# Kernel optimization log

Hardware: AMD Instinct MI355X
Metric: run time of the kernel (lower is better)

Reference implementation:

```python
import jax, jax.numpy as jnp
import numpy as np

B, N, K = 4, 8192, 16
EMBED, HID, NCLS = 64, 128, 13
EPS = 1e-5


def _bn(x, g, b):
    # BatchNorm1d in training mode: stats over all points (B*N), per channel
    m = jnp.mean(x, axis=(0, 1), keepdims=True)
    v = jnp.var(x, axis=(0, 1), keepdims=True)
    return (x - m) * jax.lax.rsqrt(v + EPS) * g + b


def _knn_idx(pos, k):
    # pos: [B,N,3] -> k nearest neighbor indices per point (self excluded)
    sq = jnp.sum(pos * pos, -1)  # [B,N]
    d2 = sq[:, :, None] + sq[:, None, :] - 2.0 * jnp.einsum('bnd,bmd->bnm', pos, pos)
    n = pos.shape[1]
    d2 = d2 + jnp.eye(n, dtype=pos.dtype) * 1e10  # mask self (loop=False)
    _, idx = jax.lax.top_k(-d2, k)  # [B,N,k]
    return idx


def _pt_conv(x, pos, idx, w_lin, w_src, w_dst, pos_w, pos_b):
    # PyG PointTransformerConv: vector attention over neighbors (incl. self loop)
    Bc = x.shape[0]
    bidx = jnp.arange(Bc)[:, None, None]
    v = x @ w_lin          # value:  lin(x)
    a_src = x @ w_src      # lin_src(x)
    a_dst = x @ w_dst      # lin_dst(x)
    vj = v[bidx, idx]                      # [B,N,k1,C]
    aj = a_src[bidx, idx]                  # [B,N,k1,C]
    pj = pos[bidx, idx]                    # [B,N,k1,3]
    delta = (pos[:, :, None, :] - pj) @ pos_w + pos_b   # pos_nn(pos_i - pos_j)
    attn = jax.nn.softmax(a_dst[:, :, None, :] - aj + delta, axis=2)
    return jnp.sum(attn * (vj + delta), axis=2)  # sum aggregation


def setup_inputs() -> dict:
    key = jax.random.key(0)
    ks = jax.random.split(key, 20)

    def w(k, fan_in, fan_out):
        return (jax.random.normal(k, (fan_in, fan_out), jnp.float32) / np.sqrt(fan_in)).astype(jnp.float32)

    inp = {
        'points': jax.random.normal(ks[0], (B, N, 3), jnp.float32),
        'embed_w1': w(ks[1], 3, EMBED), 'embed_b1': jnp.zeros((EMBED,), jnp.float32),
        'bn1_g': jnp.ones((EMBED,), jnp.float32), 'bn1_b': jnp.zeros((EMBED,), jnp.float32),
        'embed_w2': w(ks[2], EMBED, EMBED), 'embed_b2': jnp.zeros((EMBED,), jnp.float32),
        'bne_g': jnp.ones((EMBED,), jnp.float32), 'bne_b': jnp.zeros((EMBED,), jnp.float32),
        'l0_lin': w(ks[3], EMBED, HID), 'l0_src': w(ks[4], EMBED, HID), 'l0_dst': w(ks[5], EMBED, HID),
        'l0_pos_w': w(ks[6], 3, HID), 'l0_pos_b': jnp.zeros((HID,), jnp.float32),
        'l0_bn_g': jnp.ones((HID,), jnp.float32), 'l0_bn_b': jnp.zeros((HID,), jnp.float32),
        'l1_lin': w(ks[7], HID, HID), 'l1_src': w(ks[8], HID, HID), 'l1_dst': w(ks[9], HID, HID),
        'l1_pos_w': w(ks[10], 3, HID), 'l1_pos_b': jnp.zeros((HID,), jnp.float32),
        'l1_bn_g': jnp.ones((HID,), jnp.float32), 'l1_bn_b': jnp.zeros((HID,), jnp.float32),
        'dec_w1': w(ks[11], HID, HID), 'dec_b1': jnp.zeros((HID,), jnp.float32),
        'dec_bn_g': jnp.ones((HID,), jnp.float32), 'dec_bn_b': jnp.zeros((HID,), jnp.float32),
        'dec_w2': w(ks[12], HID, NCLS), 'dec_b2': jnp.zeros((NCLS,), jnp.float32),
    }
    return inp


def reference(points, embed_w1, embed_b1, bn1_g, bn1_b, embed_w2, embed_b2,
              bne_g, bne_b,
              l0_lin, l0_src, l0_dst, l0_pos_w, l0_pos_b, l0_bn_g, l0_bn_b,
              l1_lin, l1_src, l1_dst, l1_pos_w, l1_pos_b, l1_bn_g, l1_bn_b,
              dec_w1, dec_b1, dec_bn_g, dec_bn_b, dec_w2, dec_b2):
    Bc, Nc, _ = points.shape
    # embedding MLP: Linear -> BN -> ReLU -> Linear, then BN -> ReLU
    h = points @ embed_w1 + embed_b1
    h = jax.nn.relu(_bn(h, bn1_g, bn1_b))
    h = h @ embed_w2 + embed_b2
    x = jax.nn.relu(_bn(h, bne_g, bne_b))
    # kNN graph (per batch), then append self loop (add_self_loops=True)
    idx = _knn_idx(points, K)
    self_idx = jnp.broadcast_to(jnp.arange(Nc)[None, :, None], (Bc, Nc, 1))
    idxf = jnp.concatenate([idx, self_idx], axis=-1)  # [B,N,K+1]
    x = jax.nn.relu(_bn(_pt_conv(x, points, idxf, l0_lin, l0_src, l0_dst, l0_pos_w, l0_pos_b), l0_bn_g, l0_bn_b))
    x = jax.nn.relu(_bn(_pt_conv(x, points, idxf, l1_lin, l1_src, l1_dst, l1_pos_w, l1_pos_b), l1_bn_g, l1_bn_b))
    # decoder MLP (dropout = identity at inference)
    h = jax.nn.relu(_bn(x @ dec_w1 + dec_b1, dec_bn_g, dec_bn_b))
    logits = h @ dec_w2 + dec_b2  # [B,N,num_classes]
    return logits
```

## Files before the change

### kernel.cpp

```cpp
#include <hip/hip_runtime.h>
#include <math.h>

#define BB 4
#define NN 8192
#define PP 32768
#define KNN 16

typedef float f32x2 __attribute__((ext_vector_type(2)));
typedef float f32x4 __attribute__((ext_vector_type(4)));

__device__ __forceinline__ f32x2 pk_mul(f32x2 a, f32x2 b) {
  f32x2 d; asm("v_pk_mul_f32 %0, %1, %2" : "=v"(d) : "v"(a), "v"(b)); return d;
}
__device__ __forceinline__ f32x2 pk_add(f32x2 a, f32x2 b) {
  f32x2 d; asm("v_pk_add_f32 %0, %1, %2" : "=v"(d) : "v"(a), "v"(b)); return d;
}

__global__ __launch_bounds__(256) void k_embed1(const float* __restrict__ pts,
    const float* __restrict__ w1, const float* __restrict__ b1, float* __restrict__ h1)
{
  int tid = threadIdx.x;
  int c = tid & 63, g = tid >> 6;
  float wx = w1[c], wy = w1[64 + c], wz = w1[128 + c], bc = b1[c];
  int base = blockIdx.x * 256;
  #pragma unroll 4
  for (int i = 0; i < 64; ++i) {
    int p = base + g + i * 4;
    float px = pts[p*3+0], py = pts[p*3+1], pz = pts[p*3+2];
    float h = fmaf(pz, wz, fmaf(py, wy, fmaf(px, wx, bc)));
    h1[(size_t)p*64 + c] = h;
  }
}

__global__ __launch_bounds__(256) void k_prep(const float* __restrict__ pts, float* __restrict__ pp)
{
  int t = blockIdx.x * 256 + threadIdx.x;
  int b = t >> 12, m = t & 4095;
  int c = m >> 6, l = m & 63;
  int jl = b * NN + c * 128 + l;
  int jh = jl + 64;
  float xl = pts[jl*3+0], yl = pts[jl*3+1], zl = pts[jl*3+2];
  float xh = pts[jh*3+0], yh = pts[jh*3+1], zh = pts[jh*3+2];
  float wl = __fadd_rn(__fadd_rn(__fmul_rn(xl,xl), __fmul_rn(yl,yl)), __fmul_rn(zl,zl));
  float wh = __fadd_rn(__fadd_rn(__fmul_rn(xh,xh), __fmul_rn(yh,yh)), __fmul_rn(zh,zh));
  float* o = pp + (size_t)t * 8;
  *(float4*)(o + 0) = make_float4(xl, xh, yl, yh);
  *(float4*)(o + 4) = make_float4(zl, zh, wl, wh);
}

template<int C>
__global__ __launch_bounds__(256) void k_stats(const float* __restrict__ src,
    float* __restrict__ gsum, float* __restrict__ gss)
{
  constexpr int GPB = 256 / C;
  int tid = threadIdx.x;
  int c = tid % C, g = tid / C;
  float s = 0.f, ss = 0.f;
  for (int p = blockIdx.x * GPB + g; p < PP; p += gridDim.x * GPB) {
    float v = src[(size_t)p*C + c];
    s += v; ss = fmaf(v, v, ss);
  }
  __shared__ float ls[256], lq[256];
  ls[tid] = s; lq[tid] = ss;
  __syncthreads();
  if (tid < C) {
    float a = 0.f, b2 = 0.f;
    #pragma unroll
    for (int i = 0; i < GPB; ++i) { a += ls[tid + i*C]; b2 += lq[tid + i*C]; }
    atomicAdd(gsum + tid, a);
    atomicAdd(gss + tid, b2);
  }
}

__global__ void k_finalize(int C, const float* __restrict__ gsum, const float* __restrict__ gss,
    const float* __restrict__ gg, const float* __restrict__ bb,
    float* __restrict__ sc, float* __restrict__ sh)
{
  int c = threadIdx.x;
  if (c >= C) return;
  float mean = gsum[c] * (1.0f / PP);
  float var  = gss[c] * (1.0f / PP) - mean * mean;
  float s = gg[c] / sqrtf(var + 1e-5f);
  sc[c] = s;
  sh[c] = bb[c] - mean * s;
}

template<int K, int COUT>
__global__ __launch_bounds__(256) void k_proj(const float* __restrict__ in,
    const float* __restrict__ sc, const float* __restrict__ sh,
    const float* __restrict__ W0, const float* __restrict__ W1, const float* __restrict__ W2,
    const float* __restrict__ B0, const float* __restrict__ B1, const float* __restrict__ B2,
    float* __restrict__ O0, float* __restrict__ O1, float* __restrict__ O2)
{
  constexpr int PTS = 64;
  constexpr int CW = 8;
  constexpr int CG = COUT / CW;
  constexpr int PW = PTS * CG / 256;
  const float* W  = (blockIdx.y == 0) ? W0 : (blockIdx.y == 1) ? W1 : W2;
  const float* Bb = (blockIdx.y == 0) ? B0 : (blockIdx.y == 1) ? B1 : B2;
  float*       O  = (blockIdx.y == 0) ? O0 : (blockIdx.y == 1) ? O1 : O2;
  __shared__ float xs[PTS][K + 1];
  int tid = threadIdx.x;
  int pbase = blockIdx.x * PTS;
  constexpr int T4 = PTS * K / 4;
  for (int i = tid; i < T4; i += 256) {
    int p = i / (K/4), k = (i % (K/4)) * 4;
    float4 v = *(const float4*)(in + (size_t)(pbase + p)*K + k);
    v.x = fmaxf(fmaf(v.x, sc[k+0], sh[k+0]), 0.f);
    v.y = fmaxf(fmaf(v.y, sc[k+1], sh[k+1]), 0.f);
    v.z = fmaxf(fmaf(v.z, sc[k+2], sh[k+2]), 0.f);
    v.w = fmaxf(fmaf(v.w, sc[k+3], sh[k+3]), 0.f);
    xs[p][k+0] = v.x; xs[p][k+1] = v.y; xs[p][k+2] = v.z; xs[p][k+3] = v.w;
  }
  __syncthreads();
  int cg = tid % CG, pg = tid / CG;
  int c0 = cg * CW, p0 = pg * PW;
  float acc[PW][CW];
  #pragma unroll
  for (int i = 0; i < PW; ++i) {
    #pragma unroll
    for (int j = 0; j < CW; ++j) acc[i][j] = 0.f;
  }
  #pragma unroll 4
  for (int k = 0; k < K; ++k) {
    float4 wa = *(const float4*)(W + (size_t)k*COUT + c0);
    float4 wb = *(const float4*)(W + (size_t)k*COUT + c0 + 4);
    #pragma unroll
    for (int i = 0; i < PW; ++i) {
      float x = xs[p0 + i][k];
      acc[i][0] = fmaf(x, wa.x, acc[i][0]);
      acc[i][1] = fmaf(x, wa.y, acc[i][1]);
      acc[i][2] = fmaf(x, wa.z, acc[i][2]);
      acc[i][3] = fmaf(x, wa.w, acc[i][3]);
      acc[i][4] = fmaf(x, wb.x, acc[i][4]);
      acc[i][5] = fmaf(x, wb.y, acc[i][5]);
      acc[i][6] = fmaf(x, wb.z, acc[i][6]);
      acc[i][7] = fmaf(x, wb.w, acc[i][7]);
    }
  }
  float bj[CW];
  #pragma unroll
  for (int j = 0; j < CW; ++j) bj[j] = Bb ? Bb[c0 + j] : 0.f;
  #pragma unroll
  for (int i = 0; i < PW; ++i) {
    float* op = O + (size_t)(pbase + p0 + i)*COUT + c0;
    *(float4*)(op)     = make_float4(acc[i][0]+bj[0], acc[i][1]+bj[1], acc[i][2]+bj[2], acc[i][3]+bj[3]);
    *(float4*)(op + 4) = make_float4(acc[i][4]+bj[4], acc[i][5]+bj[5], acc[i][6]+bj[6], acc[i][7]+bj[7]);
  }
}

__global__ __launch_bounds__(256) void k_knn(const float* __restrict__ pp, int* __restrict__ idxout)
{
  int lane = threadIdx.x & 63;
  int wv = (blockIdx.x * 256 + threadIdx.x) >> 6;
  int b = wv >> 13, q = wv & (NN - 1);
  const float* pb = pp + (size_t)b * (NN * 4);
  const float* pq =
      nullptr;
  int qc = q >> 7, qr = q & 127;
  {
  }
  int qslot = qc * 64 + (qr & 63);
  int qh = (qr >> 6) & 1;
  const float* qpp = pb + (size_t)qslot * 8 + qh;
  float qx = qpp[0], qy = qpp[2], qz = qpp[4], qw = qpp[6];
  f32x2 qx2; qx2.x = qx; qx2.y = qx;
  f32x2 qy2; qy2.x = qy; qy2.y = qy;
  f32x2 qz2; qz2.x = qz; qz2.y = qz;
  f32x2 qw2; qw2.x = qw; qw2.y = qw;

  float lval = 3.4e38f;
  int   lidx = 0;
  float tau  = 3.4e38f;
  int l16 = lane & 15;

  auto insert = [&](unsigned long long mask, float d2v, int jbase) {
    while (mask) {
      int src = __ffsll((unsigned long long)mask) - 1;
      mask &= mask - 1;
      float v = __uint_as_float(__builtin_amdgcn_readlane(__float_as_uint(d2v), src));
      if (v < tau) {
        int jc = jbase + src;
        float pv = __shfl_up(lval, 1, 16);
        int   pi = __shfl_up(lidx, 1, 16);
        bool atpos = (l16 == 0) || (pv <= v);
        if (lval > v) {
          lval = atpos ? v  : pv;
          lidx = atpos ? jc : pi;
        }
        tau = __uint_as_float(__builtin_amdgcn_readlane(__float_as_uint(lval), 15));
      }
    }
  };

  for (int c = 0; c < 64; ++c) {
    const float* base = pb + (size_t)(c * 64 + lane) * 8;
    f32x4 A  = *(const f32x4*)(base + 0);
    f32x4 Bq = *(const f32x4*)(base + 4);
    f32x2 xs = __builtin_shufflevector(A, A, 0, 1);
    f32x2 ys = __builtin_shufflevector(A, A, 2, 3);
    f32x2 zs = __builtin_shufflevector(Bq, Bq, 0, 1);
    f32x2 ws = __builtin_shufflevector(Bq, Bq, 2, 3);
    f32x2 dot = pk_add(pk_add(pk_mul(qx2, xs), pk_mul(qy2, ys)), pk_mul(qz2, zs));
    f32x2 s2  = pk_add(qw2, ws);
    f32x2 t2  = pk_add(dot, dot);
    float d2lo = __fsub_rn(s2.x, t2.x);
    float d2hi = __fsub_rn(s2.y, t2.y);
    if (c == qc) {
      if (qr == lane)      d2lo = 3.4e38f;
      if (qr == lane + 64) d2hi = 3.4e38f;
    }
    if (c == 0) {
      float v = d2lo; int ix = lane;
      #pragma unroll
      for (int k = 2; k <= 64; k <<= 1) {
        #pragma unroll
        for (int j = k >> 1; j >= 1; j >>= 1) {
          float ov = __shfl_xor(v, j);
          int   oi = __shfl_xor(ix, j);
          bool up    = (lane & k) == 0;
          bool lower = (lane & j) == 0;
          bool lt = (ov < v) || (ov == v && oi < ix);
          bool keep = (up == lower) ? lt : !lt;
          if (keep) { v = ov; ix = oi; }
        }
      }
      lval = __shfl(v, l16);
      lidx = __shfl(ix, l16);
      tau = __uint_as_float(__builtin_amdgcn_readlane(__float_as_uint(lval), 15));
      unsigned long long mh = __ballot(d2hi < tau);
      insert(mh, d2hi, 64);
      continue;
    }
    unsigned long long ml = __ballot(d2lo < tau);
    insert(ml, d2lo, c * 128);
    unsigned long long mh = __ballot(d2hi < tau);
    insert(mh, d2hi, c * 128 + 64);
  }
  if (lane < 16) idxout[(size_t)wv * KNN + lane] = lidx;
}

__global__ __launch_bounds__(256) void k_conv(const float* __restrict__ V, const float* __restrict__ S,
    const float* __restrict__ D, const float* __restrict__ pts, const int* __restrict__ idx,
    const float* __restrict__ pw, const float* __restrict__ pbv, float* __restrict__ Y)
{
  int lane = threadIdx.x & 63;
  int wid  = (blockIdx.x * 256 + threadIdx.x) >> 6;
  int c0 = lane * 2;
  float2 w0  = *(const float2*)(pw + c0);
  float2 w1  = *(const float2*)(pw + 128 + c0);
  float2 w2  = *(const float2*)(pw + 256 + c0);
  float2 pb2 = *(const float2*)(pbv + c0);
  for (int p = wid; p < PP; p += 4096) {
    int b = p >> 13, self = p & (NN - 1);
    const float* pbase = pts + (size_t)b * NN * 3;
    float pix = pbase[self*3+0], piy = pbase[self*3+1], piz = pbase[self*3+2];
    float2 di = *(const float2*)(D + (size_t)p*128 + c0);
    float m0 = -3.4e38f, m1 = -3.4e38f, l0 = 0.f, l1 = 0.f, a0 = 0.f, a1 = 0.f;
    for (int t = 0; t < 17; ++t) {
      int j = (t < 16) ? idx[p*KNN + t] : self;
      float dx = pix - pbase[j*3+0];
      float dy = piy - pbase[j*3+1];
      float dz = piz - pbase[j*3+2];
      size_t off = ((size_t)b * NN + j) * 128 + c0;
      float2 sj = *(const float2*)(S + off);
      float2 vj = *(const float2*)(V + off);
      float de0 = fmaf(dz, w2.x, fmaf(dy, w1.x, fmaf(dx, w0.x, pb2.x)));
      float de1 = fmaf(dz, w2.y, fmaf(dy, w1.y, fmaf(dx, w0.y, pb2.y)));
      float g0 = di.x - sj.x + de0;
      float g1 = di.y - sj.y + de1;
      float mn0 = fmaxf(m0, g0), mn1 = fmaxf(m1, g1);
      float cr0 = __expf(m0 - mn0), cr1 = __expf(m1 - mn1);
      float e0  = __expf(g0 - mn0), e1  = __expf(g1 - mn1);
      l0 = fmaf(l0, cr0, e0);
      l1 = fmaf(l1, cr1, e1);
      a0 = fmaf(a0, cr0, e0 * (vj.x + de0));
      a1 = fmaf(a1, cr1, e1 * (vj.y + de1));
      m0 = mn0; m1 = mn1;
    }
    float2 o; o.x = a0 / l0; o.y = a1 / l1;
    *(float2*)(Y + (size_t)p*128 + c0) = o;
  }
}

__global__ __launch_bounds__(256) void k_dec2(const float* __restrict__ T,
    const float* __restrict__ sc, const float* __restrict__ sh,
    const float* __restrict__ W, const float* __restrict__ bias, float* __restrict__ out)
{
  __shared__ float xs[64][132];
  __shared__ float wt[13][128];
  int tid = threadIdx.x;
  int pb = blockIdx.x * 64;
  for (int i = tid; i < 13 * 128; i += 256) {
    int cls = i >> 7, k = i & 127;
    wt[cls][k] = W[k*13 + cls];
  }
  for (int i = tid; i < 64 * 32; i += 256) {
    int p = i >> 5, k = (i & 31) * 4;
    float4 v = *(const float4*)(T + (size_t)(pb + p)*128 + k);
    v.x = fmaxf(fmaf(v.x, sc[k+0], sh[k+0]), 0.f);
    v.y = fmaxf(fmaf(v.y, sc[k+1], sh[k+1]), 0.f);
    v.z = fmaxf(fmaf(v.z, sc[k+2], sh[k+2]), 0.f);
    v.w = fmaxf(fmaf(v.w, sc[k+3], sh[k+3]), 0.f);
    xs[p][k+0] = v.x; xs[p][k+1] = v.y; xs[p][k+2] = v.z; xs[p][k+3] = v.w;
  }
  __syncthreads();
  for (int o = tid; o < 64 * 13; o += 256) {
    int p = o / 13, cls = o - p * 13;
    float acc = bias[cls];
    const float4* xr = (const float4*)&xs[p][0];
    const float4* wr = (const float4*)&wt[cls][0];
    #pragma unroll 8
    for (int k4 = 0; k4 < 32; ++k4) {
      float4 a = xr[k4], w = wr[k4];
      acc = fmaf(a.x, w.x, acc);
      acc = fmaf(a.y, w.y, acc);
      acc = fmaf(a.z, w.z, acc);
      acc = fmaf(a.w, w.w, acc);
    }
    out[(size_t)(pb + p)*13 + cls] = acc;
  }
}

extern "C" void kernel_launch(void* const* d_in, const int* in_sizes, int n_in,
                              void* d_out, int out_size, void* d_ws, size_t ws_size,
                              hipStream_t stream)
{
  const float* pts      = (const float*)d_in[0];
  const float* embed_w1 = (const float*)d_in[1];
  const float* embed_b1 = (const float*)d_in[2];
  const float* bn1_g    = (const float*)d_in[3];
  const float* bn1_b    = (const float*)d_in[4];
  const float* embed_w2 = (const float*)d_in[5];
  const float* embed_b2 = (const float*)d_in[6];
  const float* bne_g    = (const float*)d_in[7];
  const float* bne_b    = (const float*)d_in[8];
  const float* l0_lin   = (const float*)d_in[9];
  const float* l0_src   = (const float*)d_in[10];
  const float* l0_dst   = (const float*)d_in[11];
  const float* l0_pos_w = (const float*)d_in[12];
  const float* l0_pos_b = (const float*)d_in[13];
  const float* l0_bn_g  = (const float*)d_in[14];
  const float* l0_bn_b  = (const float*)d_in[15];
  const float* l1_lin   = (const float*)d_in[16];
  const float* l1_src   = (const float*)d_in[17];
  const float* l1_dst   = (const float*)d_in[18];
  const float* l1_pos_w = (const float*)d_in[19];
  const float* l1_pos_b = (const float*)d_in[20];
  const float* l1_bn_g  = (const float*)d_in[21];
  const float* l1_bn_b  = (const float*)d_in[22];
  const float* dec_w1   = (const float*)d_in[23];
  const float* dec_b1   = (const float*)d_in[24];
  const float* dec_bn_g = (const float*)d_in[25];
  const float* dec_bn_b = (const float*)d_in[26];
  const float* dec_w2   = (const float*)d_in[27];
  const float* dec_b2   = (const float*)d_in[28];

  char* ws = (char*)d_ws;
  const size_t MB = 1024 * 1024;
  float* h1  = (float*)(ws + 0);
  float* h2  = (float*)(ws + 8*MB);
  int*   idx = (int*)  (ws + 16*MB);
  float* v0  = (float*)(ws + 18*MB);
  float* s0  = (float*)(ws + 34*MB);
  float* d0  = (float*)(ws + 50*MB);
  float* y0  = (float*)(ws + 66*MB);
  float* y1  = (float*)(ws + 82*MB);
  float* tt  = (float*)(ws + 0);
  float* pairs8 = (float*)(ws + 18*MB);
  float* st  = (float*)(ws + 98*MB);
  float *sum1=st+0,    *ss1=st+64,   *sc1=st+128,  *sh1=st+192;
  float *sum2=st+256,  *ss2=st+320,  *sc2=st+384,  *sh2=st+448;
  float *sum3=st+512,  *ss3=st+640,  *sc3=st+768,  *sh3=st+896;
  float *sum4=st+1024, *ss4=st+1152, *sc4=st+1280, *sh4=st+1408;
  float *sum5=st+1536, *ss5=st+1664, *sc5=st+1792, *sh5=st+1920;

  hipMemsetAsync(st, 0, 2048 * sizeof(float), stream);

  k_prep<<<64, 256, 0, stream>>>(pts, pairs8);
  k_knn<<<8192, 256, 0, stream>>>(pairs8, idx);

  k_embed1<<<128, 256, 0, stream>>>(pts, embed_w1, embed_b1, h1);
  k_stats<64><<<128, 256, 0, stream>>>(h1, sum1, ss1);
  k_finalize<<<1, 64, 0, stream>>>(64, sum1, ss1, bn1_g, bn1_b, sc1, sh1);
  k_proj<64,64><<<dim3(512,1), 256, 0, stream>>>(h1, sc1, sh1,
      embed_w2, embed_w2, embed_w2, embed_b2, embed_b2, embed_b2, h2, h2, h2);
  k_stats<64><<<128, 256, 0, stream>>>(h2, sum2, ss2);
  k_finalize<<<1, 64, 0, stream>>>(64, sum2, ss2, bne_g, bne_b, sc2, sh2);

  k_proj<64,128><<<dim3(512,3), 256, 0, stream>>>(h2, sc2, sh2,
      l0_lin, l0_src, l0_dst, nullptr, nullptr, nullptr, v0, s0, d0);
  k_conv<<<1024, 256, 0, stream>>>(v0, s0, d0, pts, idx, l0_pos_w, l0_pos_b, y0);
  k_stats<128><<<128, 256, 0, stream>>>(y0, sum3, ss3);
  k_finalize<<<1, 128, 0, stream>>>(128, sum3, ss3, l0_bn_g, l0_bn_b, sc3, sh3);

  k_proj<128,128><<<dim3(512,3), 256, 0, stream>>>(y0, sc3, sh3,
      l1_lin, l1_src, l1_dst, nullptr, nullptr, nullptr, v0, s0, d0);
  k_conv<<<1024, 256, 0, stream>>>(v0, s0, d0, pts, idx, l1_pos_w, l1_pos_b, y1);
  k_stats<128><<<128, 256, 0, stream>>>(y1, sum4, ss4);
  k_finalize<<<1, 128, 0, stream>>>(128, sum4, ss4, l1_bn_g, l1_bn_b, sc4, sh4);

  k_proj<128,128><<<dim3(512,1), 256, 0, stream>>>(y1, sc4, sh4,
      dec_w1, dec_w1, dec_w1, dec_b1, dec_b1, dec_b1, tt, tt, tt);
  k_stats<128><<<128, 256, 0, stream>>>(tt, sum5, ss5);
  k_finalize<<<1, 128, 0, stream>>>(128, sum5, ss5, dec_bn_g, dec_bn_b, sc5, sh5);
  k_dec2<<<512, 256, 0, stream>>>(tt, sc5, sh5, dec_w2, dec_b2, (float*)d_out);
}
```

Before: 732.6 us.

## Process four kNN queries per wavefront with 16-lane groups; widen stats grid

The kNN kernel now packs four queries per 64-lane wavefront, one per 16-lane group. Each group scans 32-point chunks, and the prep kernel re-tiles the candidate pairs to match that chunk size. Insertion into each group's sorted top-16 list uses ds_permute/bpermute in place of per-lane readlane, so all four groups insert in parallel, and the launch uses a quarter of the blocks. The goal is to cut the serial insertion and full-wave scan overhead per query, at the cost of more loop iterations and more divergence across groups. The BN stats kernels also get four times as many blocks to raise parallelism in the reductions.

```diff
diff --git a/kernel.cpp b/kernel.cpp
--- a/kernel.cpp
+++ b/kernel.cpp
@@ -36,9 +36,9 @@
 {
   int t = blockIdx.x * 256 + threadIdx.x;
   int b = t >> 12, m = t & 4095;
-  int c = m >> 6, l = m & 63;
-  int jl = b * NN + c * 128 + l;
-  int jh = jl + 64;
+  int c = m >> 4, l = m & 15;
+  int jl = b * NN + c * 32 + l;
+  int jh = jl + 16;
   float xl = pts[jl*3+0], yl = pts[jl*3+1], zl = pts[jl*3+2];
   float xh = pts[jh*3+0], yh = pts[jh*3+1], zh = pts[jh*3+2];
   float wl = __fadd_rn(__fadd_rn(__fmul_rn(xl,xl), __fmul_rn(yl,yl)), __fmul_rn(zl,zl));
@@ -149,54 +149,104 @@
   }
 }
 
-__global__ __launch_bounds__(256) void k_knn(const float* __restrict__ pp, int* __restrict__ idxout)
-{
-  int lane = threadIdx.x & 63;
-  int wv = (blockIdx.x * 256 + threadIdx.x) >> 6;
-  int b = wv >> 13, q = wv & (NN - 1);
+__global__ __launch_bounds__(256, 8) void k_knn(const float* __restrict__ pp, int* __restrict__ idxout)
+{
+  int tid = threadIdx.x;
+  int lane = tid & 63;
+  int l16 = lane & 15;
+  int g64 = lane & 48;
+  int wv = (blockIdx.x * 256 + tid) >> 6;
+  int b  = wv >> 11;
+  int qbase = (wv * 4) & (NN - 1);
+  int qc = qbase >> 5;
+  int qr = (qbase & 31) + (lane >> 4);
   const float* pb = pp + (size_t)b * (NN * 4);
-  const float* pq =
-      nullptr;
-  int qc = q >> 7, qr = q & 127;
+
+  float qx, qy, qz, qw;
   {
-  }
-  int qslot = qc * 64 + (qr & 63);
-  int qh = (qr >> 6) & 1;
-  const float* qpp = pb + (size_t)qslot * 8 + qh;
-  float qx = qpp[0], qy = qpp[2], qz = qpp[4], qw = qpp[6];
+    int qslot = qc * 16 + (qr & 15);
+    int qh = (qr >> 4) & 1;
+    const float* qp = pb + (size_t)qslot * 8 + qh;
+    qx = qp[0]; qy = qp[2]; qz = qp[4]; qw = qp[6];
+  }
   f32x2 qx2; qx2.x = qx; qx2.y = qx;
   f32x2 qy2; qy2.x = qy; qy2.y = qy;
   f32x2 qz2; qz2.x = qz; qz2.y = qz;
   f32x2 qw2; qw2.x = qw; qw2.y = qw;
 
+  int addr_push = (lane + 1) << 2;
+  int addr_tau  = (g64 + 15) << 2;
+
   float lval = 3.4e38f;
   int   lidx = 0;
   float tau  = 3.4e38f;
-  int l16 = lane & 15;
-
-  auto insert = [&](unsigned long long mask, float d2v, int jbase) {
-    while (mask) {
-      int src = __ffsll((unsigned long long)mask) - 1;
-      mask &= mask - 1;
-      float v = __uint_as_float(__builtin_amdgcn_readlane(__float_as_uint(d2v), src));
-      if (v < tau) {
+
+  auto half_pass = [&](float d2, int jbase) {
+    unsigned long long bal = __ballot(d2 < tau);
+    if (bal) {
+      unsigned slice = (unsigned)(bal >> g64) & 0xffffu;
+      while (__ballot(slice != 0)) {
+        bool live = slice != 0;
+        int src = __ffs((int)slice) - 1;
+        slice &= slice - 1;
+        int ab = (g64 + (src & 15)) << 2;
+        float v = __uint_as_float(__builtin_amdgcn_ds_bpermute(ab, __float_as_uint(d2)));
+        if (!live) v = 3.4e38f;
         int jc = jbase + src;
-        float pv = __shfl_up(lval, 1, 16);
-        int   pi = __shfl_up(lidx, 1, 16);
+        float pv = __uint_as_float(__builtin_amdgcn_ds_permute(addr_push, __float_as_uint(lval)));
+        int   pi = __builtin_amdgcn_ds_permute(addr_push, lidx);
         bool atpos = (l16 == 0) || (pv <= v);
         if (lval > v) {
           lval = atpos ? v  : pv;
           lidx = atpos ? jc : pi;
         }
-        tau = __uint_as_float(__builtin_amdgcn_readlane(__float_as_uint(lval), 15));
       }
+      tau = __uint_as_float(__builtin_amdgcn_ds_bpermute(addr_tau, __float_as_uint(lval)));
     }
   };
 
-  for (int c = 0; c < 64; ++c) {
-    const float* base = pb + (size_t)(c * 64 + lane) * 8;
-    f32x4 A  = *(const f32x4*)(base + 0);
-    f32x4 Bq = *(const f32x4*)(base + 4);
+  const float* cp = pb + (size_t)l16 * 8;
+
+  {
+    f32x4 A  = *(const f32x4*)(cp + 0);
+    f32x4 Bq = *(const f32x4*)(cp + 4);
+    cp += 128;
+    f32x2 xs = __builtin_shufflevector(A, A, 0, 1);
+    f32x2 ys = __builtin_shufflevector(A, A, 2, 3);
+    f32x2 zs = __builtin_shufflevector(Bq, Bq, 0, 1);
+    f32x2 ws = __builtin_shufflevector(Bq, Bq, 2, 3);
+    f32x2 dot = pk_add(pk_add(pk_mul(qx2, xs), pk_mul(qy2, ys)), pk_mul(qz2, zs));
+    f32x2 s2  = pk_add(qw2, ws);
+    f32x2 t2  = pk_add(dot, dot);
+    float d2lo = __fsub_rn(s2.x, t2.x);
+    float d2hi = __fsub_rn(s2.y, t2.y);
+    if (qc == 0) {
+      bool lo = qr < 16;
+      int  tl = lo ? qr : qr - 16;
+      if (l16 == tl) { if (lo) d2lo = 3.4e38f; else d2hi = 3.4e38f; }
+    }
+    float v = d2lo; int ix = l16;
+    #pragma unroll
+    for (int k = 2; k <= 16; k <<= 1) {
+      #pragma unroll
+      for (int j = k >> 1; j >= 1; j >>= 1) {
+        float ov = __shfl_xor(v, j, 16);
+        int   oi = __shfl_xor(ix, j, 16);
+        bool up    = (l16 & k) == 0;
+        bool lower = (l16 & j) == 0;
+        bool lt = (ov < v) || (ov == v && oi < ix);
+        if ((up == lower) ? lt : !lt) { v = ov; ix = oi; }
+      }
+    }
+    lval = v; lidx = ix;
+    tau = __uint_as_float(__builtin_amdgcn_ds_bpermute(addr_tau, __float_as_uint(lval)));
+    half_pass(d2hi, 16);
+  }
+
+  for (int c = 1; c < 256; ++c) {
+    f32x4 A  = *(const f32x4*)(cp + 0);
+    f32x4 Bq = *(const f32x4*)(cp + 4);
+    cp += 128;
     f32x2 xs = __builtin_shufflevector(A, A, 0, 1);
     f32x2 ys = __builtin_shufflevector(A, A, 2, 3);
     f32x2 zs = __builtin_shufflevector(Bq, Bq, 0, 1);
@@ -207,37 +257,15 @@
     float d2lo = __fsub_rn(s2.x, t2.x);
     float d2hi = __fsub_rn(s2.y, t2.y);
     if (c == qc) {
-      if (qr == lane)      d2lo = 3.4e38f;
-      if (qr == lane + 64) d2hi = 3.4e38f;
-    }
-    if (c == 0) {
-      float v = d2lo; int ix = lane;
-      #pragma unroll
-      for (int k = 2; k <= 64; k <<= 1) {
-        #pragma unroll
-        for (int j = k >> 1; j >= 1; j >>= 1) {
-          float ov = __shfl_xor(v, j);
-          int   oi = __shfl_xor(ix, j);
-          bool up    = (lane & k) == 0;
-          bool lower = (lane & j) == 0;
-          bool lt = (ov < v) || (ov == v && oi < ix);
-          bool keep = (up == lower) ? lt : !lt;
-          if (keep) { v = ov; ix = oi; }
-        }
-      }
-      lval = __shfl(v, l16);
-      lidx = __shfl(ix, l16);
-      tau = __uint_as_float(__builtin_amdgcn_readlane(__float_as_uint(lval), 15));
-      unsigned long long mh = __ballot(d2hi < tau);
-      insert(mh, d2hi, 64);
-      continue;
-    }
-    unsigned long long ml = __ballot(d2lo < tau);
-    insert(ml, d2lo, c * 128);
-    unsigned long long mh = __ballot(d2hi < tau);
-    insert(mh, d2hi, c * 128 + 64);
-  }
-  if (lane < 16) idxout[(size_t)wv * KNN + lane] = lidx;
+      bool lo = qr < 16;
+      int  tl = lo ? qr : qr - 16;
+      if (l16 == tl) { if (lo) d2lo = 3.4e38f; else d2hi = 3.4e38f; }
+    }
+    half_pass(d2lo, c * 32);
+    half_pass(d2hi, c * 32 + 16);
+  }
+
+  idxout[(size_t)wv * 64 + lane] = lidx;
 }
 
 __global__ __launch_bounds__(256) void k_conv(const float* __restrict__ V, const float* __restrict__ S,
@@ -378,31 +406,31 @@
   hipMemsetAsync(st, 0, 2048 * sizeof(float), stream);
 
   k_prep<<<64, 256, 0, stream>>>(pts, pairs8);
-  k_knn<<<8192, 256, 0, stream>>>(pairs8, idx);
+  k_knn<<<2048, 256, 0, stream>>>(pairs8, idx);
 
   k_embed1<<<128, 256, 0, stream>>>(pts, embed_w1, embed_b1, h1);
-  k_stats<64><<<128, 256, 0, stream>>>(h1, sum1, ss1);
+  k_stats<64><<<512, 256, 0, stream>>>(h1, sum1, ss1);
   k_finalize<<<1, 64, 0, stream>>>(64, sum1, ss1, bn1_g, bn1_b, sc1, sh1);
   k_proj<64,64><<<dim3(512,1), 256, 0, stream>>>(h1, sc1, sh1,
       embed_w2, embed_w2, embed_w2, embed_b2, embed_b2, embed_b2, h2, h2, h2);
-  k_stats<64><<<128, 256, 0, stream>>>(h2, sum2, ss2);
+  k_stats<64><<<512, 256, 0, stream>>>(h2, sum2, ss2);
   k_finalize<<<1, 64, 0, stream>>>(64, sum2, ss2, bne_g, bne_b, sc2, sh2);
 
   k_proj<64,128><<<dim3(512,3), 256, 0, stream>>>(h2, sc2, sh2,
       l0_lin, l0_src, l0_dst, nullptr, nullptr, nullptr, v0, s0, d0);
   k_conv<<<1024, 256, 0, stream>>>(v0, s0, d0, pts, idx, l0_pos_w, l0_pos_b, y0);
-  k_stats<128><<<128, 256, 0, stream>>>(y0, sum3, ss3);
+  k_stats<128><<<512, 256, 0, stream>>>(y0, sum3, ss3);
   k_finalize<<<1, 128, 0, stream>>>(128, sum3, ss3, l0_bn_g, l0_bn_b, sc3, sh3);
 
   k_proj<128,128><<<dim3(512,3), 256, 0, stream>>>(y0, sc3, sh3,
       l1_lin, l1_src, l1_dst, nullptr, nullptr, nullptr, v0, s0, d0);
   k_conv<<<1024, 256, 0, stream>>>(v0, s0, d0, pts, idx, l1_pos_w, l1_pos_b, y1);
-  k_stats<128><<<128, 256, 0, stream>>>(y1, sum4, ss4);
+  k_stats<128><<<512, 256, 0, stream>>>(y1, sum4, ss4);
   k_finalize<<<1, 128, 0, stream>>>(128, sum4, ss4, l1_bn_g, l1_bn_b, sc4, sh4);
 
   k_proj<128,128><<<dim3(512,1), 256, 0, stream>>>(y1, sc4, sh4,
       dec_w1, dec_w1, dec_w1, dec_b1, dec_b1, dec_b1, tt, tt, tt);
-  k_stats<128><<<128, 256, 0, stream>>>(tt, sum5, ss5);
+  k_stats<128><<<512, 256, 0, stream>>>(tt, sum5, ss5);
   k_finalize<<<1, 128, 0, stream>>>(128, sum5, ss5, dec_bn_g, dec_bn_b, sc5, sh5);
   k_dec2<<<512, 256, 0, stream>>>(tt, sc5, sh5, dec_w2, dec_b2, (float*)d_out);
 }
```

After: 689.7 us. -5.9%, faster.
